# Kernel optimization log

Measured on AMD Instinct MI355X. Metric: run time of the kernel, lower is better.

## Reference

```python
import jax, jax.numpy as jnp
import numpy as np

S, B, D, H = 2048, 64, 128, 128


def setup_inputs() -> dict:
    key = jax.random.key(0)
    ks = jax.random.split(key, 7)
    scale = 1.0 / np.sqrt(H)
    return {
        "input": jax.random.normal(ks[0], (S, B, D), dtype=jnp.float32),
        "time": jax.random.uniform(ks[1], (S, B, 1), dtype=jnp.float32),
        "W_ih": jax.random.normal(ks[2], (4 * H, D), dtype=jnp.float32) * scale,
        "W_hh": jax.random.normal(ks[3], (4 * H, H), dtype=jnp.float32) * scale,
        "b": jax.random.normal(ks[4], (4 * H,), dtype=jnp.float32) * scale,
        "w_t": jax.random.uniform(ks[5], (H,), dtype=jnp.float32),
        "b_t": jax.random.uniform(ks[6], (H,), dtype=jnp.float32),
    }


def reference(input, time, W_ih, W_hh, b, w_t, b_t):
    # ReverseLSTMLayer: run a time-conditioned LSTM cell over REVERSED time steps,
    # then re-reverse the stacked outputs. state starts at zeros (state=None).
    Bsz = input.shape[1]
    Hd = W_hh.shape[1]

    def step(state, xt):
        x, t = xt  # x: [B, D], t: [B, 1]
        h, c = state
        gates = x @ W_ih.T + h @ W_hh.T + b  # [B, 4H]
        i_, f_, g_, o_ = jnp.split(gates, 4, axis=-1)
        i_ = jax.nn.sigmoid(i_)
        f_ = jax.nn.sigmoid(f_)
        g_ = jnp.tanh(g_)
        o_ = jax.nn.sigmoid(o_)
        # learned exponential time decay on the carried cell state (T-LSTM style)
        decay = jnp.exp(-jax.nn.relu(t * w_t + b_t))  # [B, H]
        c = f_ * c * decay + i_ * g_
        h = o_ * jnp.tanh(c)
        return (h, c), h

    init = (jnp.zeros((Bsz, Hd), input.dtype), jnp.zeros((Bsz, Hd), input.dtype))
    # iterate over reversed sequence, then reverse outputs back
    (h, c), ys_rev = jax.lax.scan(step, init, (input[::-1], time[::-1]))
    outputs = ys_rev[::-1]  # [S, B, H]
    return outputs, (h, c)
```

## Files before the change

### kernel.cpp

```cpp
#include <hip/hip_runtime.h>

#define S_LEN 2048
#define B_SZ  64
#define D_IN  128
#define H_SZ  128
#define G4    512

typedef __attribute__((ext_vector_type(4))) float     floatx4;
typedef __attribute__((ext_vector_type(8))) _Float16  half8;
typedef __attribute__((ext_vector_type(4))) _Float16  half4;
typedef __attribute__((ext_vector_type(2))) _Float16  half2_t;

template<int CTRL>
__device__ __forceinline__ float qperm(float v) {
  return __int_as_float(
      __builtin_amdgcn_mov_dpp(__float_as_int(v), CTRL, 0xF, 0xF, true));
}

template<int P>
__device__ __forceinline__ half2_t h2ext(half8 v) {
  return __builtin_shufflevector(v, v, 2 * P, 2 * P + 1);
}

__device__ __forceinline__ void lds_barrier() {
  asm volatile("s_waitcnt lgkmcnt(0)\n\ts_barrier" ::: "memory");
}

__global__ __launch_bounds__(256) void gx_gemm(
    const float* __restrict__ X,
    const float* __restrict__ Wih,
    const float* __restrict__ bias,
    _Float16* __restrict__ gx)
{
  __shared__ _Float16 Wl[128][136];
  const int tid  = threadIdx.x;
  const int lane = tid & 63;
  const int wv   = tid >> 6;
  const int b    = blockIdx.y;
  const int T0   = blockIdx.x * 256;
  const int m    = lane & 15;
  const int q    = lane >> 4;

  const float LOG2E = 1.4426950408889634f;

  half8 afrag[4][4];
  #pragma unroll
  for (int rg = 0; rg < 4; ++rg) {
    const int t = T0 + rg * 64 + wv * 16 + m;
    const float* xrow = X + ((size_t)t * B_SZ + b) * D_IN;
    #pragma unroll
    for (int kf = 0; kf < 4; ++kf) {
      const int k0 = kf * 32 + q * 8;
      floatx4 v0 = *(const floatx4*)(xrow + k0);
      floatx4 v1 = *(const floatx4*)(xrow + k0 + 4);
      half8 a;
      a[0] = (_Float16)v0.x; a[1] = (_Float16)v0.y;
      a[2] = (_Float16)v0.z; a[3] = (_Float16)v0.w;
      a[4] = (_Float16)v1.x; a[5] = (_Float16)v1.y;
      a[6] = (_Float16)v1.z; a[7] = (_Float16)v1.w;
      afrag[rg][kf] = a;
    }
  }

  for (int nc = 0; nc < 4; ++nc) {
    const float sc = (nc == 2) ? (-2.0f * LOG2E) : (-LOG2E);
    __syncthreads();
    for (int i = tid; i < 128 * 32; i += 256) {
      const int row = i >> 5;
      const int c4  = (i & 31) * 4;
      floatx4 v = *(const floatx4*)(Wih + ((size_t)nc * 128 + row) * D_IN + c4);
      Wl[row][c4 + 0] = (_Float16)v.x;
      Wl[row][c4 + 1] = (_Float16)v.y;
      Wl[row][c4 + 2] = (_Float16)v.z;
      Wl[row][c4 + 3] = (_Float16)v.w;
    }
    __syncthreads();

    #pragma unroll
    for (int nt = 0; nt < 8; ++nt) {
      const int n0  = nc * 128 + nt * 16;
      const int nlo = nt * 16 + m;
      const float bv = bias[n0 + m];
      half8 bfrag[4];
      #pragma unroll
      for (int kf = 0; kf < 4; ++kf)
        bfrag[kf] = *(const half8*)(&Wl[nlo][kf * 32 + q * 8]);
      #pragma unroll
      for (int rg = 0; rg < 4; ++rg) {
        floatx4 acc = {bv, bv, bv, bv};
        #pragma unroll
        for (int kf = 0; kf < 4; ++kf)
          acc = __builtin_amdgcn_mfma_f32_16x16x32_f16(afrag[rg][kf],
                                                       bfrag[kf], acc, 0, 0, 0);
        const int tbase = T0 + rg * 64 + wv * 16 + q * 4;
        half4 hv;
        hv[0] = (_Float16)(acc[0] * sc);
        hv[1] = (_Float16)(acc[1] * sc);
        hv[2] = (_Float16)(acc[2] * sc);
        hv[3] = (_Float16)(acc[3] * sc);
        *(half4*)(gx + ((size_t)b * G4 + n0 + m) * S_LEN + tbase) = hv;
      }
    }
  }
}

__device__ __forceinline__ float fd(half2_t a, half2_t b, float c) {
  return __builtin_amdgcn_fdot2(a, b, c, false);
}

__device__ __forceinline__ half8 wcvt(const float* __restrict__ p, float sc) {
  floatx4 v0 = *(const floatx4*)p;
  floatx4 v1 = *(const floatx4*)(p + 4);
  half8 h;
  h[0] = (_Float16)(v0.x * sc); h[1] = (_Float16)(v0.y * sc);
  h[2] = (_Float16)(v0.z * sc); h[3] = (_Float16)(v0.w * sc);
  h[4] = (_Float16)(v1.x * sc); h[5] = (_Float16)(v1.y * sc);
  h[6] = (_Float16)(v1.z * sc); h[7] = (_Float16)(v1.w * sc);
  return h;
}

#define PIN_WEIGHTS()                                                         \
  asm volatile(""                                                             \
               : "+v"(w00), "+v"(w01), "+v"(w02), "+v"(w03),                  \
                 "+v"(w10), "+v"(w11), "+v"(w12), "+v"(w13),                  \
                 "+v"(w20), "+v"(w21), "+v"(w22), "+v"(w23),                  \
                 "+v"(w30), "+v"(w31), "+v"(w32), "+v"(w33),                  \
                 "+v"(wt), "+v"(bt))

#define DOT8(HV, WA, WB, WC, WD)                                              \
  {                                                                           \
    q0a = fd(h2ext<0>(HV), h2ext<0>(WA), q0a);                                \
    q1a = fd(h2ext<0>(HV), h2ext<0>(WB), q1a);                                \
    q2a = fd(h2ext<0>(HV), h2ext<0>(WC), q2a);                                \
    q3a = fd(h2ext<0>(HV), h2ext<0>(WD), q3a);                                \
    q0a = fd(h2ext<1>(HV), h2ext<1>(WA), q0a);                                \
    q1a = fd(h2ext<1>(HV), h2ext<1>(WB), q1a);                                \
    q2a = fd(h2ext<1>(HV), h2ext<1>(WC), q2a);                                \
    q3a = fd(h2ext<1>(HV), h2ext<1>(WD), q3a);                                \
    q0b = fd(h2ext<2>(HV), h2ext<2>(WA), q0b);                                \
    q1b = fd(h2ext<2>(HV), h2ext<2>(WB), q1b);                                \
    q2b = fd(h2ext<2>(HV), h2ext<2>(WC), q2b);                                \
    q3b = fd(h2ext<2>(HV), h2ext<2>(WD), q3b);                                \
    q0b = fd(h2ext<3>(HV), h2ext<3>(WA), q0b);                                \
    q1b = fd(h2ext<3>(HV), h2ext<3>(WB), q1b);                                \
    q2b = fd(h2ext<3>(HV), h2ext<3>(WC), q2b);                                \
    q3b = fd(h2ext<3>(HV), h2ext<3>(WD), q3b);                                \
  }

#define GATE(HR, GXV, TMV, CVAR, HVAR)                                        \
  {                                                                           \
    half8 hv0 = *(const half8*)((HR) + 0 * 32 + tt * 8);                      \
    half8 hv1 = *(const half8*)((HR) + 1 * 32 + tt * 8);                      \
    half8 hv2 = *(const half8*)((HR) + 2 * 32 + tt * 8);                      \
    half8 hv3 = *(const half8*)((HR) + 3 * 32 + tt * 8);                      \
    asm volatile("" : "+v"(hv0), "+v"(hv1), "+v"(hv2), "+v"(hv3));            \
    float q0a = 0.f, q0b = 0.f, q1a = 0.f, q1b = 0.f;                         \
    float q2a = 0.f, q2b = 0.f, q3a = 0.f, q3b = 0.f;                         \
    PIN_WEIGHTS();                                                            \
    DOT8(hv0, w00, w10, w20, w30);                                            \
    PIN_WEIGHTS();                                                            \
    DOT8(hv1, w01, w11, w21, w31);                                            \
    PIN_WEIGHTS();                                                            \
    DOT8(hv2, w02, w12, w22, w32);                                            \
    PIN_WEIGHTS();                                                            \
    DOT8(hv3, w03, w13, w23, w33);                                            \
    float a0 = q0a + q0b, a1 = q1a + q1b, a2 = q2a + q2b, a3 = q3a + q3b;     \
    a0 += qperm<0xB1>(a0); a1 += qperm<0xB1>(a1);                             \
    a2 += qperm<0xB1>(a2); a3 += qperm<0xB1>(a3);                             \
    a0 += qperm<0x4E>(a0); a1 += qperm<0x4E>(a1);                             \
    a2 += qperm<0x4E>(a2); a3 += qperm<0x4E>(a3);                             \
    float pre = (tt & 1) ? ((tt & 2) ? a3 : a1) : ((tt & 2) ? a2 : a0);       \
    pre += (GXV);            \
    const float e  = __builtin_amdgcn_exp2f(pre);                             \
    const float v  = fmaf(am, __builtin_amdgcn_rcpf(1.0f + e), aa);           \
    float z = fmaf((TMV), wt, bt);                  \
    z = fminf(z, 0.0f);                                   \
    const float d  = __builtin_amdgcn_exp2f(z);                               \
    const float p2 = qperm<0x4E>(v);                                          \
    const float fv = (tt == 1) ? v : p2;                                      \
    const float r  = odd ? fv * (d * (CVAR)) : v * p2;                        \
    const float cn = r + qperm<0xB1>(r);                                      \
    (CVAR) = cn;                                                              \
    const float e2 = __builtin_amdgcn_exp2f(-2.0f * LOG2E * cn);              \
    const float th = fmaf(2.0f, __builtin_amdgcn_rcpf(1.0f + e2), -1.0f);     \
    (HVAR) = v * th;                                                          \
  }

#define SUB(K, TMV, RP, WP)                                                   \
  {                                                                           \
    const float g0 = (float)cur8[K];                                          \
    float h0;                                                                 \
    GATE(&hbuf[RP][0], g0, (TMV), c, h0);                                     \
    if (tt == 3) {                                                            \
      hbuf[WP][col] = (_Float16)h0;                                           \
      const int tcur = blk * 8 + K;                                           \
      out[((size_t)tcur << 13) + bH + col] = h0;                              \
      if (tcur == 0) {                                                        \
        float* hf = out + (size_t)S_LEN * B_SZ * H_SZ;                        \
        hf[bH + col] = h0;                                                    \
        hf[(size_t)B_SZ * H_SZ + bH + col] = c;                               \
      }                                                                       \
    }                                                                         \
    lds_barrier();                                                            \
  }

__global__ __launch_bounds__(512)
__attribute__((amdgpu_waves_per_eu(2, 2)))
void lstm_rev(
    const _Float16* __restrict__ gx,
    const float* __restrict__ timep,
    const float* __restrict__ Whh,
    const float* __restrict__ w_tp,
    const float* __restrict__ b_tp,
    float* __restrict__ out)
{
  __shared__ __align__(16) _Float16 hbuf[2][H_SZ];
  __shared__ __align__(16) float    tml[S_LEN];
  const int tid = threadIdx.x;
  const int b   = blockIdx.x;
  const int tt  = tid & 3;
  const int col = tid >> 2;
  const int j   = tt * 128 + col;

  const float LOG2E = 1.4426950408889634f;

  #pragma unroll
  for (int k = 0; k < 4; ++k) {
    const int idx = tid + k * 512;
    tml[idx] = timep[(idx << 6) + b];
  }

  half8 w00, w01, w02, w03, w10, w11, w12, w13;
  half8 w20, w21, w22, w23, w30, w31, w32, w33;
  {
    const float s1 = -LOG2E, s2 = -2.0f * LOG2E;
    const float* r0 = Whh + (size_t)(0 * 128 + col) * H_SZ + tt * 8;
    const float* r1 = Whh + (size_t)(1 * 128 + col) * H_SZ + tt * 8;
    const float* r2 = Whh + (size_t)(2 * 128 + col) * H_SZ + tt * 8;
    const float* r3 = Whh + (size_t)(3 * 128 + col) * H_SZ + tt * 8;
    w00 = wcvt(r0 +  0, s1); w01 = wcvt(r0 + 32, s1);
    w02 = wcvt(r0 + 64, s1); w03 = wcvt(r0 + 96, s1);
    w10 = wcvt(r1 +  0, s1); w11 = wcvt(r1 + 32, s1);
    w12 = wcvt(r1 + 64, s1); w13 = wcvt(r1 + 96, s1);
    w20 = wcvt(r2 +  0, s2); w21 = wcvt(r2 + 32, s2);
    w22 = wcvt(r2 + 64, s2); w23 = wcvt(r2 + 96, s2);
    w30 = wcvt(r3 +  0, s1); w31 = wcvt(r3 + 32, s1);
    w32 = wcvt(r3 + 64, s1); w33 = wcvt(r3 + 96, s1);
  }

  float wt = -LOG2E * w_tp[col];
  float bt = -LOG2E * b_tp[col];
  const float am  = (tt == 2) ? 2.0f : 1.0f;
  const float aa  = (tt == 2) ? -1.0f : 0.0f;
  const bool  odd = (tt & 1) != 0;

  if (tid < 2 * H_SZ) ((_Float16*)hbuf)[tid] = (_Float16)0.0f;
  __syncthreads();

  const _Float16* gxr = gx + ((size_t)b * G4 + j) * S_LEN;
  const size_t bH = (size_t)b * H_SZ;

  half8 cur8 = *(const half8*)(gxr + 255 * 8);
  half8 nxt8 = *(const half8*)(gxr + 254 * 8);

  float c = 0.0f;

  for (int blk = 255; blk >= 0; --blk) {
    PIN_WEIGHTS();
    const int pfb = (blk >= 2) ? blk - 2 : 0;
    half8 fut8 = *(const half8*)(gxr + pfb * 8);
    const floatx4 tmA = *(const floatx4*)(&tml[blk * 8 + 4]);
    const floatx4 tmB = *(const floatx4*)(&tml[blk * 8 + 0]);

    SUB(7, tmA.w, 0, 1)
    SUB(6, tmA.z, 1, 0)
    SUB(5, tmA.y, 0, 1)
    SUB(4, tmA.x, 1, 0)
    SUB(3, tmB.w, 0, 1)
    SUB(2, tmB.z, 1, 0)
    SUB(1, tmB.y, 0, 1)
    SUB(0, tmB.x, 1, 0)

    cur8 = nxt8;
    nxt8 = fut8;
  }
}

extern "C" void kernel_launch(void* const* d_in, const int* in_sizes, int n_in,
                              void* d_out, int out_size, void* d_ws, size_t ws_size,
                              hipStream_t stream) {
  const float* input = (const float*)d_in[0];
  const float* timep = (const float*)d_in[1];
  const float* W_ih  = (const float*)d_in[2];
  const float* W_hh  = (const float*)d_in[3];
  const float* bias  = (const float*)d_in[4];
  const float* w_t   = (const float*)d_in[5];
  const float* b_t   = (const float*)d_in[6];
  float* out = (float*)d_out;

  _Float16* gx = (_Float16*)d_ws;

  gx_gemm<<<dim3(S_LEN / 256, B_SZ), dim3(256), 0, stream>>>(
      input, W_ih, bias, gx);

  lstm_rev<<<dim3(B_SZ), dim3(512), 0, stream>>>(
      gx, timep, W_hh, w_t, b_t, out);
}
```

Measured before the change: 1.271 ms.

## Fuse input GEMM and reverse LSTM into one producer-consumer kernel with flags

Merges the input-projection GEMM and the recurrent LSTM kernel into a single launch of 128 blocks. 64 producer blocks compute gate pre-activations chunk by chunk in reverse time order and publish per-chunk completion flags. 64 consumer blocks run the recurrence and spin-wait on those flags before prefetching each chunk. The intent is to overlap the GEMM with the serial recurrence and remove a kernel launch boundary. In exchange it adds a memset per call, atomic polling, and relies on all 128 blocks being co-resident to avoid deadlock.

```diff
diff --git a/kernel.cpp b/kernel.cpp
--- a/kernel.cpp
+++ b/kernel.cpp
@@ -24,84 +24,6 @@
 
 __device__ __forceinline__ void lds_barrier() {
   asm volatile("s_waitcnt lgkmcnt(0)\n\ts_barrier" ::: "memory");
-}
-
-__global__ __launch_bounds__(256) void gx_gemm(
-    const float* __restrict__ X,
-    const float* __restrict__ Wih,
-    const float* __restrict__ bias,
-    _Float16* __restrict__ gx)
-{
-  __shared__ _Float16 Wl[128][136];
-  const int tid  = threadIdx.x;
-  const int lane = tid & 63;
-  const int wv   = tid >> 6;
-  const int b    = blockIdx.y;
-  const int T0   = blockIdx.x * 256;
-  const int m    = lane & 15;
-  const int q    = lane >> 4;
-
-  const float LOG2E = 1.4426950408889634f;
-
-  half8 afrag[4][4];
-  #pragma unroll
-  for (int rg = 0; rg < 4; ++rg) {
-    const int t = T0 + rg * 64 + wv * 16 + m;
-    const float* xrow = X + ((size_t)t * B_SZ + b) * D_IN;
-    #pragma unroll
-    for (int kf = 0; kf < 4; ++kf) {
-      const int k0 = kf * 32 + q * 8;
-      floatx4 v0 = *(const floatx4*)(xrow + k0);
-      floatx4 v1 = *(const floatx4*)(xrow + k0 + 4);
-      half8 a;
-      a[0] = (_Float16)v0.x; a[1] = (_Float16)v0.y;
-      a[2] = (_Float16)v0.z; a[3] = (_Float16)v0.w;
-      a[4] = (_Float16)v1.x; a[5] = (_Float16)v1.y;
-      a[6] = (_Float16)v1.z; a[7] = (_Float16)v1.w;
-      afrag[rg][kf] = a;
-    }
-  }
-
-  for (int nc = 0; nc < 4; ++nc) {
-    const float sc = (nc == 2) ? (-2.0f * LOG2E) : (-LOG2E);
-    __syncthreads();
-    for (int i = tid; i < 128 * 32; i += 256) {
-      const int row = i >> 5;
-      const int c4  = (i & 31) * 4;
-      floatx4 v = *(const floatx4*)(Wih + ((size_t)nc * 128 + row) * D_IN + c4);
-      Wl[row][c4 + 0] = (_Float16)v.x;
-      Wl[row][c4 + 1] = (_Float16)v.y;
-      Wl[row][c4 + 2] = (_Float16)v.z;
-      Wl[row][c4 + 3] = (_Float16)v.w;
-    }
-    __syncthreads();
-
-    #pragma unroll
-    for (int nt = 0; nt < 8; ++nt) {
-      const int n0  = nc * 128 + nt * 16;
-      const int nlo = nt * 16 + m;
-      const float bv = bias[n0 + m];
-      half8 bfrag[4];
-      #pragma unroll
-      for (int kf = 0; kf < 4; ++kf)
-        bfrag[kf] = *(const half8*)(&Wl[nlo][kf * 32 + q * 8]);
-      #pragma unroll
-      for (int rg = 0; rg < 4; ++rg) {
-        floatx4 acc = {bv, bv, bv, bv};
-        #pragma unroll
-        for (int kf = 0; kf < 4; ++kf)
-          acc = __builtin_amdgcn_mfma_f32_16x16x32_f16(afrag[rg][kf],
-                                                       bfrag[kf], acc, 0, 0, 0);
-        const int tbase = T0 + rg * 64 + wv * 16 + q * 4;
-        half4 hv;
-        hv[0] = (_Float16)(acc[0] * sc);
-        hv[1] = (_Float16)(acc[1] * sc);
-        hv[2] = (_Float16)(acc[2] * sc);
-        hv[3] = (_Float16)(acc[3] * sc);
-        *(half4*)(gx + ((size_t)b * G4 + n0 + m) * S_LEN + tbase) = hv;
-      }
-    }
-  }
 }
 
 __device__ __forceinline__ float fd(half2_t a, half2_t b, float c) {
@@ -117,6 +39,104 @@
   h[4] = (_Float16)(v1.x * sc); h[5] = (_Float16)(v1.y * sc);
   h[6] = (_Float16)(v1.z * sc); h[7] = (_Float16)(v1.w * sc);
   return h;
+}
+
+__device__ int g_flags[512];
+
+union SharedU {
+  _Float16 Wl[128][136];
+  struct {
+    _Float16 hbuf[2][H_SZ];
+    float    tml[S_LEN];
+  } l;
+};
+
+
+__device__ void gx_role(int b, const float* __restrict__ X,
+                        const float* __restrict__ Wih,
+                        const float* __restrict__ bias,
+                        _Float16* __restrict__ gx,
+                        SharedU* su, int* __restrict__ flags)
+{
+  const int tid  = threadIdx.x;
+  const int lane = tid & 63;
+  const int wv   = tid >> 6;
+  const int m    = lane & 15;
+  const int q    = lane >> 4;
+  const float LOG2E = 1.4426950408889634f;
+
+  for (int chunk = 7; chunk >= 0; --chunk) {
+    const int T0 = chunk * 256;
+
+    half8 afrag[4][4];
+    if (wv < 4) {
+      #pragma unroll
+      for (int rg = 0; rg < 4; ++rg) {
+        const int t = T0 + rg * 64 + wv * 16 + m;
+        const float* xrow = X + ((size_t)t * B_SZ + b) * D_IN;
+        #pragma unroll
+        for (int kf = 0; kf < 4; ++kf) {
+          const int k0 = kf * 32 + q * 8;
+          floatx4 v0 = *(const floatx4*)(xrow + k0);
+          floatx4 v1 = *(const floatx4*)(xrow + k0 + 4);
+          half8 a;
+          a[0] = (_Float16)v0.x; a[1] = (_Float16)v0.y;
+          a[2] = (_Float16)v0.z; a[3] = (_Float16)v0.w;
+          a[4] = (_Float16)v1.x; a[5] = (_Float16)v1.y;
+          a[6] = (_Float16)v1.z; a[7] = (_Float16)v1.w;
+          afrag[rg][kf] = a;
+        }
+      }
+    }
+
+    for (int nc = 0; nc < 4; ++nc) {
+      const float sc = (nc == 2) ? (-2.0f * LOG2E) : (-LOG2E);
+      __syncthreads();
+      for (int i = tid; i < 128 * 32; i += 512) {
+        const int row = i >> 5;
+        const int c4  = (i & 31) * 4;
+        floatx4 v =
+            *(const floatx4*)(Wih + ((size_t)nc * 128 + row) * D_IN + c4);
+        su->Wl[row][c4 + 0] = (_Float16)v.x;
+        su->Wl[row][c4 + 1] = (_Float16)v.y;
+        su->Wl[row][c4 + 2] = (_Float16)v.z;
+        su->Wl[row][c4 + 3] = (_Float16)v.w;
+      }
+      __syncthreads();
+
+      if (wv < 4) {
+        #pragma unroll
+        for (int nt = 0; nt < 8; ++nt) {
+          const int n0  = nc * 128 + nt * 16;
+          const int nlo = nt * 16 + m;
+          const float bv = bias[n0 + m];
+          half8 bfrag[4];
+          #pragma unroll
+          for (int kf = 0; kf < 4; ++kf)
+            bfrag[kf] = *(const half8*)(&su->Wl[nlo][kf * 32 + q * 8]);
+          #pragma unroll
+          for (int rg = 0; rg < 4; ++rg) {
+            floatx4 acc = {bv, bv, bv, bv};
+            #pragma unroll
+            for (int kf = 0; kf < 4; ++kf)
+              acc = __builtin_amdgcn_mfma_f32_16x16x32_f16(
+                  afrag[rg][kf], bfrag[kf], acc, 0, 0, 0);
+            const int tbase = T0 + rg * 64 + wv * 16 + q * 4;
+            half4 hv;
+            hv[0] = (_Float16)(acc[0] * sc);
+            hv[1] = (_Float16)(acc[1] * sc);
+            hv[2] = (_Float16)(acc[2] * sc);
+            hv[3] = (_Float16)(acc[3] * sc);
+            *(half4*)(gx + ((size_t)b * G4 + n0 + m) * S_LEN + tbase) = hv;
+          }
+        }
+      }
+    }
+
+    __threadfence();
+    __syncthreads();
+    if (tid == 0) atomicAdd(&flags[(b << 3) + chunk], 1);
+  }
 }
 
 #define PIN_WEIGHTS()                                                         \
@@ -204,20 +224,27 @@
     lds_barrier();                                                            \
   }
 
-__global__ __launch_bounds__(512)
-__attribute__((amdgpu_waves_per_eu(2, 2)))
-void lstm_rev(
-    const _Float16* __restrict__ gx,
-    const float* __restrict__ timep,
-    const float* __restrict__ Whh,
-    const float* __restrict__ w_tp,
-    const float* __restrict__ b_tp,
-    float* __restrict__ out)
+#define WAITCH(CH)                                                            \
+  {                                                                           \
+    if (tid == 0) {                                                           \
+      while (atomicAdd(&flags[(b << 3) + (CH)], 0) == 0)                      \
+        __builtin_amdgcn_s_sleep(2);                                          \
+    }                                                                         \
+    __syncthreads();                                                          \
+    __threadfence();                                                          \
+  }
+
+__device__ void lstm_role(int b, const _Float16* __restrict__ gx,
+                          const float* __restrict__ timep,
+                          const float* __restrict__ Whh,
+                          const float* __restrict__ w_tp,
+                          const float* __restrict__ b_tp,
+                          float* __restrict__ out,
+                          SharedU* su, int* __restrict__ flags)
 {
-  __shared__ __align__(16) _Float16 hbuf[2][H_SZ];
-  __shared__ __align__(16) float    tml[S_LEN];
+  _Float16 (*hbuf)[H_SZ] = su->l.hbuf;
+  float* tml = su->l.tml;
   const int tid = threadIdx.x;
-  const int b   = blockIdx.x;
   const int tt  = tid & 3;
   const int col = tid >> 2;
   const int j   = tt * 128 + col;
@@ -257,6 +284,9 @@
   if (tid < 2 * H_SZ) ((_Float16*)hbuf)[tid] = (_Float16)0.0f;
   __syncthreads();
 
+  int have = 7;
+  WAITCH(7);
+
   const _Float16* gxr = gx + ((size_t)b * G4 + j) * S_LEN;
   const size_t bH = (size_t)b * H_SZ;
 
@@ -267,7 +297,9 @@
 
   for (int blk = 255; blk >= 0; --blk) {
     PIN_WEIGHTS();
-    const int pfb = (blk >= 2) ? blk - 2 : 0;
+    const int pfb  = (blk >= 2) ? blk - 2 : 0;
+    const int need = pfb >> 5;
+    if (need != have) { WAITCH(need); have = need; }
     half8 fut8 = *(const half8*)(gxr + pfb * 8);
     const floatx4 tmA = *(const floatx4*)(&tml[blk * 8 + 4]);
     const floatx4 tmB = *(const floatx4*)(&tml[blk * 8 + 0]);
@@ -283,6 +315,28 @@
 
     cur8 = nxt8;
     nxt8 = fut8;
+  }
+}
+
+__global__ __launch_bounds__(512)
+__attribute__((amdgpu_waves_per_eu(2, 2)))
+void fused(const float* __restrict__ X,
+           const float* __restrict__ timep,
+           const float* __restrict__ Wih,
+           const float* __restrict__ Whh,
+           const float* __restrict__ bias,
+           const float* __restrict__ w_tp,
+           const float* __restrict__ b_tp,
+           _Float16* __restrict__ gx,
+           int* __restrict__ flags,
+           float* __restrict__ out)
+{
+  __shared__ __align__(16) SharedU su;
+  const int bx = blockIdx.x;
+  if (bx < 64) {
+    gx_role(bx, X, Wih, bias, gx, &su, flags);
+  } else {
+    lstm_role(bx - 64, gx, timep, Whh, w_tp, b_tp, out, &su, flags);
   }
 }
 
@@ -300,9 +354,12 @@
 
   _Float16* gx = (_Float16*)d_ws;
 
-  gx_gemm<<<dim3(S_LEN / 256, B_SZ), dim3(256), 0, stream>>>(
-      input, W_ih, bias, gx);
-
-  lstm_rev<<<dim3(B_SZ), dim3(512), 0, stream>>>(
-      gx, timep, W_hh, w_t, b_t, out);
-}
+  static int* flags_ptr = nullptr;
+  if (!flags_ptr)
+    (void)hipGetSymbolAddress((void**)&flags_ptr, HIP_SYMBOL(g_flags));
+
+  hipMemsetAsync(flags_ptr, 0, 512 * sizeof(int), stream);
+
+  fused<<<dim3(128), dim3(512), 0, stream>>>(
+      input, timep, W_ih, W_hh, bias, w_t, b_t, gx, flags_ptr, out);
+}
```

After: 1.358 ms. +6.8%, slower.
